# Performance work log

Measured on AMD Instinct MI355X. Metric: run time of the kernel, lower is better.

The kernel has to match this reference:

```python
import jax, jax.numpy as jnp
import numpy as np

NW, OBS, HS, HS2, HM, CTX, ACT = 2048, 512, 512, 512, 256, 128, 18


def setup_inputs() -> dict:
    key = jax.random.key(0)
    ks = jax.random.split(key, 20)
    s = 0.02  # small init so tanh/softmax/sigmoid stay in sane range
    f32 = jnp.float32
    return {
        "obs": jax.random.normal(ks[0], (NW, 1, OBS), f32),
        "hidden_memory": jax.random.normal(ks[1], (1, NW, HM), f32),
        # fnn: Linear(obs_size, hidden_size)
        "W1": (jax.random.normal(ks[2], (HS, OBS), f32) * s),
        "b1": jnp.zeros((HS,), f32),
        # context: Linear(hidden_memory_size + 1, context_size)
        "Wc": (jax.random.normal(ks[3], (CTX, HM + 1), f32) * s),
        "bc": jnp.zeros((CTX,), f32),
        # attention: Linear(context_size, 1)
        "Wa": (jax.random.normal(ks[4], (1, CTX), f32) * s),
        "ba": jnp.zeros((1,), f32),
        # GRU(input=1, hidden=HM)
        "W_ih": (jax.random.normal(ks[5], (3 * HM, 1), f32) * s),
        "b_ih": jnp.zeros((3 * HM,), f32),
        "W_hh": (jax.random.normal(ks[6], (3 * HM, HM), f32) * s),
        "b_hh": jnp.zeros((3 * HM,), f32),
        # fnn2: Linear(hidden_size + hidden_memory_size, hidden_size_2)
        "W2": (jax.random.normal(ks[7], (HS2, HS + HM), f32) * s),
        "b2": jnp.zeros((HS2,), f32),
        # actor / critic heads
        "Wact": (jax.random.normal(ks[8], (ACT, HS2), f32) * s),
        "bact": jnp.zeros((ACT,), f32),
        "Wcrit": (jax.random.normal(ks[9], (1, HS2), f32) * s),
        "bcrit": jnp.zeros((1,), f32),
    }


def reference(obs, hidden_memory, W1, b1, Wc, bc, Wa, ba,
              W_ih, b_ih, W_hh, b_hh, W2, b2, Wact, bact, Wcrit, bcrit):
    # obs: [NW, 1, OBS], hidden_memory: [1, NW, HM]
    feat = jax.nn.relu(jnp.einsum('bto,ho->bth', obs, W1) + b1)  # [NW,1,HS]

    # context: Linear([obs_scalar, hidden_memory]) + tanh.
    # Split the (HM+1)-dim contraction: col 0 multiplies the obs scalar,
    # cols 1: contract with the broadcast hidden memory (same math as the
    # torch cat + Linear, without materializing the [NW,1,OBS,HM+1] tensor).
    h = jnp.swapaxes(hidden_memory, 0, 1)                        # [NW,1,HM]
    h_term = jnp.einsum('btm,cm->btc', h, Wc[:, 1:]) + bc        # [NW,1,CTX]
    ctx = jnp.tanh(obs[..., None] * Wc[:, 0] + h_term[:, :, None, :])  # [NW,1,OBS,CTX]

    # attention: Linear(CTX -> 1) then softmax over the obs dimension (dim=-2
    # of [...,OBS,1] == OBS after squeeze)
    alog = jnp.einsum('btoc,c->bto', ctx, Wa[0]) + ba[0]         # [NW,1,OBS]
    attn = jax.nn.softmax(alog, axis=-1)
    dset = jnp.sum(attn * obs, axis=-1, keepdims=True)           # [NW,1,1]

    # single-step GRU (torch gate ordering: r, z, n)
    x = dset[:, 0, :]                                            # [NW,1]
    hp = hidden_memory[0]                                        # [NW,HM]
    gi = x @ W_ih.T + b_ih                                       # [NW,3HM]
    gh = hp @ W_hh.T + b_hh
    ir, iz, inn = jnp.split(gi, 3, axis=-1)
    hr, hz, hn = jnp.split(gh, 3, axis=-1)
    r = jax.nn.sigmoid(ir + hr)
    z = jax.nn.sigmoid(iz + hz)
    n = jnp.tanh(inn + r * hn)
    hnew = (1.0 - z) * n + z * hp                                # [NW,HM]

    out = jnp.concatenate([feat[:, 0, :], hnew], axis=-1)        # [NW,HS+HM]
    out = jax.nn.relu(out @ W2.T + b2)                           # [NW,HS2]
    logits = out @ Wact.T + bact                                 # [NW,ACT]
    action = jax.random.categorical(jax.random.key(42), logits)  # [NW]
    log_prob = jax.nn.log_softmax(logits)[jnp.arange(logits.shape[0]), action]
    value = out @ Wcrit.T + bcrit                                # [NW,1]
    return (action, value, log_prob)
```

## Files before the change

kernel.cpp:

```cpp
#include <hip/hip_runtime.h>
#include <stdint.h>

#define NW   2048
#define OBS  512
#define HS   512
#define HS2  512
#define HM   256
#define CTX  128
#define ACT  18

#define K2LE 2.8853900817779268f

#define W1T_OFF   0
#define WCT_OFF   262144
#define WHHT_OFF  294912
#define W2T_OFF   491520
#define FEAT_OFF  884736
#define HTERM_OFF 1933312
#define GATES_OFF 2195456
#define OUT2_OFF  2195456
#define HNEW_OFF  3768320

#if __has_builtin(__builtin_amdgcn_exp2f)
#define EXP2F(x) __builtin_amdgcn_exp2f(x)
#else
#define EXP2F(x) exp2f(x)
#endif
#if __has_builtin(__builtin_amdgcn_rcpf)
#define RCPF(x) __builtin_amdgcn_rcpf(x)
#else
#define RCPF(x) (1.0f/(x))
#endif

#define TFR(x0, x1, R) { x0 += x1; x1 = (x1 << R) | (x1 >> (32 - R)); x1 ^= x0; }

__device__ __forceinline__ void threefry_0_42(uint32_t x0, uint32_t x1,
                                              uint32_t& o0, uint32_t& o1) {
    const uint32_t ks0 = 0u;
    const uint32_t ks1 = 42u;
    const uint32_t ks2 = 0x1BD11BDAu ^ ks0 ^ ks1;
    x0 += ks0; x1 += ks1;
    TFR(x0, x1, 13) TFR(x0, x1, 15) TFR(x0, x1, 26) TFR(x0, x1, 6)
    x0 += ks1; x1 += ks2 + 1u;
    TFR(x0, x1, 17) TFR(x0, x1, 29) TFR(x0, x1, 16) TFR(x0, x1, 24)
    x0 += ks2; x1 += ks0 + 2u;
    TFR(x0, x1, 13) TFR(x0, x1, 15) TFR(x0, x1, 26) TFR(x0, x1, 6)
    x0 += ks0; x1 += ks1 + 3u;
    TFR(x0, x1, 17) TFR(x0, x1, 29) TFR(x0, x1, 16) TFR(x0, x1, 24)
    x0 += ks1; x1 += ks2 + 4u;
    TFR(x0, x1, 13) TFR(x0, x1, 15) TFR(x0, x1, 26) TFR(x0, x1, 6)
    x0 += ks2; x1 += ks0 + 5u;
    o0 = x0; o1 = x1;
}

__device__ __forceinline__ float gumbel_ra(int row, int a) {
    uint32_t n = (uint32_t)(row * ACT + a);
    uint32_t o0, o1;
    threefry_0_42(0u, n, o0, o1);
    uint32_t bits = o0 ^ o1;
    uint32_t fb = (bits >> 9) | 0x3F800000u;
    float f = __uint_as_float(fb) - 1.0f;
    const float tiny = 1.17549435e-38f;
    float u = (f < tiny) ? tiny : f;
    return -logf(-logf(u));
}

__device__ __forceinline__ float fast_tanh(float x) {
    float e = __expf(2.0f * x);
    return 1.0f - 2.0f / (e + 1.0f);
}
__device__ __forceinline__ float fast_sig(float x) {
    return 1.0f / (1.0f + __expf(-x));
}
__device__ __forceinline__ void fma4(float4& a, float s, const float4 w) {
    a.x = fmaf(s, w.x, a.x); a.y = fmaf(s, w.y, a.y);
    a.z = fmaf(s, w.z, a.z); a.w = fmaf(s, w.w, a.w);
}

__global__ __launch_bounds__(256) void transpose_weights(
    const float* __restrict__ W1, const float* __restrict__ Wc,
    const float* __restrict__ Whh, const float* __restrict__ W2,
    float* __restrict__ ws)
{
    int b = blockIdx.x;
    const float* src; float* dst; int ld, off, R, it, jt;
    if (b < 256)      { src = W1;  dst = ws + W1T_OFF;  ld = 512; off = 0; it = b >> 4; jt = b & 15; R = 512; }
    else if (b < 288) { b -= 256; src = Wc;  dst = ws + WCT_OFF;  ld = 257; off = 1; it = b >> 3; jt = b & 7;  R = 128; }
    else if (b < 480) { b -= 288; src = Whh; dst = ws + WHHT_OFF; ld = 256; off = 0; it = b / 8;  jt = b % 8;  R = 768; }
    else              { b -= 480; src = W2;  dst = ws + W2T_OFF;  ld = 768; off = 0; it = b / 24; jt = b % 24; R = 512; }
    __shared__ float t[32][33];
    const int tx = threadIdx.x & 31, ty = threadIdx.x >> 5;
    const int i0 = it * 32, j0 = jt * 32;
    #pragma unroll
    for (int q = 0; q < 4; ++q)
        t[ty + 8 * q][tx] = src[(i0 + ty + 8 * q) * ld + off + j0 + tx];
    __syncthreads();
    #pragma unroll
    for (int q = 0; q < 4; ++q)
        dst[(j0 + ty + 8 * q) * R + i0 + tx] = t[tx][ty + 8 * q];
}

__global__ __launch_bounds__(256) void gemm_bcast(
    const float* __restrict__ obs, const float* __restrict__ hmem,
    const float* __restrict__ b1,  const float* __restrict__ bc,
    const float* __restrict__ bhh, float* __restrict__ ws)
{
    __shared__ float s_act[16 * 768];
    float4* P = (float4*)s_act;

    int bid = blockIdx.x;
    const float* A; int lda; const float4* Bt4; int NQ, K, kshift;
    const float* bias; float* C; int ldc; float scale; int act; int rowb, colb;
    if (bid < 512) {
        rowb = bid >> 2; colb = bid & 3;
        A = obs; lda = 512; Bt4 = (const float4*)(ws + W1T_OFF); NQ = 128; K = 512; kshift = 7;
        bias = b1; C = ws + FEAT_OFF; ldc = 512; scale = 1.0f; act = 1;
    } else if (bid < 640) {
        rowb = bid - 512; colb = 0;
        A = hmem; lda = 256; Bt4 = (const float4*)(ws + WCT_OFF); NQ = 32; K = 256; kshift = 6;
        bias = bc; C = ws + HTERM_OFF; ldc = 128; scale = K2LE; act = 0;
    } else {
        int i = bid - 640; rowb = i / 6; colb = i - rowb * 6;
        A = hmem; lda = 256; Bt4 = (const float4*)(ws + WHHT_OFF); NQ = 192; K = 256; kshift = 6;
        bias = bhh; C = ws + GATES_OFF; ldc = 768; scale = 1.0f; act = 0;
    }
    const int m0 = rowb * 16;
    const int kq4 = K >> 2;

    for (int i = threadIdx.x; i < 16 * kq4; i += 256) {
        int r = i >> kshift, kq = i & (kq4 - 1);
        *(float4*)&s_act[r * K + kq * 4] =
            *(const float4*)&A[(size_t)(m0 + r) * lda + kq * 4];
    }
    __syncthreads();

    const int lane = threadIdx.x & 63, wv = threadIdx.x >> 6;
    const int kq2 = lane & 1, c4l = lane >> 1;
    const int kslice = K >> 3;
    const int k0 = (wv * 2 + kq2) * kslice;
    const int cq = colb * 32 + c4l;

    float4 acc[16];
    #pragma unroll
    for (int r = 0; r < 16; ++r) acc[r] = make_float4(0.f, 0.f, 0.f, 0.f);

    #pragma unroll 2
    for (int kk = k0; kk < k0 + kslice; kk += 4) {
        float4 w0 = Bt4[(kk + 0) * NQ + cq];
        float4 w1 = Bt4[(kk + 1) * NQ + cq];
        float4 w2 = Bt4[(kk + 2) * NQ + cq];
        float4 w3 = Bt4[(kk + 3) * NQ + cq];
        #pragma unroll
        for (int r = 0; r < 16; ++r) {
            float4 o = *(const float4*)&s_act[r * K + kk];
            fma4(acc[r], o.x, w0); fma4(acc[r], o.y, w1);
            fma4(acc[r], o.z, w2); fma4(acc[r], o.w, w3);
        }
    }
    #pragma unroll
    for (int r = 0; r < 16; ++r) {
        acc[r].x += __shfl_xor(acc[r].x, 1);
        acc[r].y += __shfl_xor(acc[r].y, 1);
        acc[r].z += __shfl_xor(acc[r].z, 1);
        acc[r].w += __shfl_xor(acc[r].w, 1);
    }
    __syncthreads();
    if (kq2 == 0) {
        #pragma unroll
        for (int r = 0; r < 16; ++r) P[(r * 4 + wv) * 32 + c4l] = acc[r];
    }
    __syncthreads();
    const float4* bias4 = (const float4*)bias;
    for (int s = threadIdx.x; s < 512; s += 256) {
        int r = s >> 5, c = s & 31;
        float4 p0 = P[(r * 4 + 0) * 32 + c];
        float4 p1 = P[(r * 4 + 1) * 32 + c];
        float4 p2 = P[(r * 4 + 2) * 32 + c];
        float4 p3 = P[(r * 4 + 3) * 32 + c];
        float4 bb = bias4[colb * 32 + c];
        float4 v;
        v.x = (p0.x + p1.x + p2.x + p3.x + bb.x) * scale;
        v.y = (p0.y + p1.y + p2.y + p3.y + bb.y) * scale;
        v.z = (p0.z + p1.z + p2.z + p3.z + bb.z) * scale;
        v.w = (p0.w + p1.w + p2.w + p3.w + bb.w) * scale;
        if (act) {
            v.x = fmaxf(v.x, 0.f); v.y = fmaxf(v.y, 0.f);
            v.z = fmaxf(v.z, 0.f); v.w = fmaxf(v.w, 0.f);
        }
        *(float4*)&C[(size_t)(m0 + r) * ldc + (colb * 32 + c) * 4] = v;
    }
}

__global__ __launch_bounds__(512) void attn_gru_kernel(
    const float* __restrict__ obs,  const float* __restrict__ hmem,
    const float* __restrict__ Wc,   const float* __restrict__ Wa,
    const float* __restrict__ ba,   const float* __restrict__ W_ih,
    const float* __restrict__ b_ih, float* __restrict__ ws)
{
    __shared__ float s_obs[8][512];
    __shared__ float s_ht[8][128];
    __shared__ float s_alog[8][512];
    __shared__ float s_wc0[128], s_wa2[128];
    __shared__ float s_x[8];

    const int tid = threadIdx.x;
    const int row0 = blockIdx.x * 8;
    const float* hterm = ws + HTERM_OFF;
    const float* gates = ws + GATES_OFF;
    float* hnew = ws + HNEW_OFF;

    for (int i = tid; i < 1024; i += 512) {
        int r = i >> 7, kq = i & 127;
        *(float4*)&s_obs[r][kq * 4] =
            *(const float4*)&obs[(size_t)(row0 + r) * 512 + kq * 4];
    }
    if (tid < 256) {
        int r = tid >> 5, kq = tid & 31;
        *(float4*)&s_ht[r][kq * 4] =
            *(const float4*)&hterm[(size_t)(row0 + r) * 128 + kq * 4];
    }
    if (tid < 128) {
        s_wc0[tid] = K2LE * Wc[tid * (HM + 1)];
        s_wa2[tid] = 2.0f * Wa[tid];
    }
    __syncthreads();

    {
        const float ba0 = ba[0];
        const int o = tid;
        float ob[8], acA[8];
        #pragma unroll
        for (int r = 0; r < 8; ++r) { ob[r] = s_obs[r][o]; acA[r] = 0.f; }
        float swa = 0.f;
        for (int c = 0; c < 128; c += 4) {
            float4 v = *(const float4*)&s_wa2[c];
            swa += v.x + v.y + v.z + v.w;
        }
        swa *= 0.5f;
        for (int c4 = 0; c4 < 32; ++c4) {
            float4 wc = *(const float4*)&s_wc0[c4 * 4];
            float4 wa = *(const float4*)&s_wa2[c4 * 4];
            #pragma unroll
            for (int r = 0; r < 8; ++r) {
                float4 ht = *(const float4*)&s_ht[r][c4 * 4];
                float t0 = fmaf(ob[r], wc.x, ht.x);
                acA[r] = fmaf(wa.x, RCPF(EXP2F(t0) + 1.f), acA[r]);
                float t1 = fmaf(ob[r], wc.y, ht.y);
                acA[r] = fmaf(wa.y, RCPF(EXP2F(t1) + 1.f), acA[r]);
                float t2 = fmaf(ob[r], wc.z, ht.z);
                acA[r] = fmaf(wa.z, RCPF(EXP2F(t2) + 1.f), acA[r]);
                float t3 = fmaf(ob[r], wc.w, ht.w);
                acA[r] = fmaf(wa.w, RCPF(EXP2F(t3) + 1.f), acA[r]);
            }
        }
        #pragma unroll
        for (int r = 0; r < 8; ++r) s_alog[r][o] = ba0 + swa - acA[r];
    }
    __syncthreads();

    {
        const int wv = tid >> 6, lane = tid & 63;
        const int r = wv;
        float m = -1e30f;
        for (int o = lane; o < 512; o += 64) m = fmaxf(m, s_alog[r][o]);
        #pragma unroll
        for (int d = 32; d >= 1; d >>= 1) m = fmaxf(m, __shfl_xor(m, d));
        float se = 0.f, sw = 0.f;
        for (int o = lane; o < 512; o += 64) {
            float e = __expf(s_alog[r][o] - m);
            se += e; sw += e * s_obs[r][o];
        }
        #pragma unroll
        for (int d = 32; d >= 1; d >>= 1) { se += __shfl_xor(se, d); sw += __shfl_xor(sw, d); }
        if (lane == 0) s_x[r] = sw / se;
    }
    __syncthreads();

    #pragma unroll
    for (int q = 0; q < 4; ++q) {
        int e = tid + q * 512;
        int r = e >> 8, j = e & 255;
        int grow = row0 + r;
        float g0 = gates[(size_t)grow * 768 + j];
        float g1 = gates[(size_t)grow * 768 + 256 + j];
        float g2 = gates[(size_t)grow * 768 + 512 + j];
        float hp = hmem[(size_t)grow * 256 + j];
        float x  = s_x[r];
        float rg = fast_sig(fmaf(x, W_ih[j], b_ih[j]) + g0);
        float zg = fast_sig(fmaf(x, W_ih[256 + j], b_ih[256 + j]) + g1);
        float ng = fast_tanh(fmaf(x, W_ih[512 + j], b_ih[512 + j]) + rg * g2);
        hnew[(size_t)grow * 256 + j] = (1.0f - zg) * ng + zg * hp;
    }
}

__global__ __launch_bounds__(256) void gemm_out2(
    const float* __restrict__ b2, float* __restrict__ ws)
{
    __shared__ float s_act[16 * 768];
    float4* P = (float4*)s_act;

    const int bid = blockIdx.x;
    const int rowb = bid >> 2, colb = bid & 3;
    const int m0 = rowb * 16;
    const float* feat = ws + FEAT_OFF;
    const float* hnew = ws + HNEW_OFF;
    const float4* Bt4 = (const float4*)(ws + W2T_OFF);
    float* C = ws + OUT2_OFF;

    for (int i = threadIdx.x; i < 16 * 192; i += 256) {
        int r = i / 192, kq = i - r * 192;
        float4 v = (kq < 128)
            ? *(const float4*)&feat[(size_t)(m0 + r) * 512 + kq * 4]
            : *(const float4*)&hnew[(size_t)(m0 + r) * 256 + (kq - 128) * 4];
        *(float4*)&s_act[r * 768 + kq * 4] = v;
    }
    __syncthreads();

    const int lane = threadIdx.x & 63, wv = threadIdx.x >> 6;
    const int kq2 = lane & 1, c4l = lane >> 1;
    const int kslice = 96;
    const int k0 = (wv * 2 + kq2) * kslice;
    const int cq = colb * 32 + c4l;

    float4 acc[16];
    #pragma unroll
    for (int r = 0; r < 16; ++r) acc[r] = make_float4(0.f, 0.f, 0.f, 0.f);

    #pragma unroll 2
    for (int kk = k0; kk < k0 + kslice; kk += 4) {
        float4 w0 = Bt4[(kk + 0) * 128 + cq];
        float4 w1 = Bt4[(kk + 1) * 128 + cq];
        float4 w2 = Bt4[(kk + 2) * 128 + cq];
        float4 w3 = Bt4[(kk + 3) * 128 + cq];
        #pragma unroll
        for (int r = 0; r < 16; ++r) {
            float4 o = *(const float4*)&s_act[r * 768 + kk];
            fma4(acc[r], o.x, w0); fma4(acc[r], o.y, w1);
            fma4(acc[r], o.z, w2); fma4(acc[r], o.w, w3);
        }
    }
    #pragma unroll
    for (int r = 0; r < 16; ++r) {
        acc[r].x += __shfl_xor(acc[r].x, 1);
        acc[r].y += __shfl_xor(acc[r].y, 1);
        acc[r].z += __shfl_xor(acc[r].z, 1);
        acc[r].w += __shfl_xor(acc[r].w, 1);
    }
    __syncthreads();
    if (kq2 == 0) {
        #pragma unroll
        for (int r = 0; r < 16; ++r) P[(r * 4 + wv) * 32 + c4l] = acc[r];
    }
    __syncthreads();
    const float4* bias4 = (const float4*)b2;
    for (int s = threadIdx.x; s < 512; s += 256) {
        int r = s >> 5, c = s & 31;
        float4 p0 = P[(r * 4 + 0) * 32 + c];
        float4 p1 = P[(r * 4 + 1) * 32 + c];
        float4 p2 = P[(r * 4 + 2) * 32 + c];
        float4 p3 = P[(r * 4 + 3) * 32 + c];
        float4 bb = bias4[colb * 32 + c];
        float4 v;
        v.x = fmaxf(p0.x + p1.x + p2.x + p3.x + bb.x, 0.f);
        v.y = fmaxf(p0.y + p1.y + p2.y + p3.y + bb.y, 0.f);
        v.z = fmaxf(p0.z + p1.z + p2.z + p3.z + bb.z, 0.f);
        v.w = fmaxf(p0.w + p1.w + p2.w + p3.w + bb.w, 0.f);
        *(float4*)&C[(size_t)(m0 + r) * 512 + (colb * 32 + c) * 4] = v;
    }
}

__global__ __launch_bounds__(512) void heads_kernel(
    const float* __restrict__ Wact,  const float* __restrict__ bact,
    const float* __restrict__ Wcrit, const float* __restrict__ bcrit,
    const float* __restrict__ ws,    float* __restrict__ out)
{
    const int wv = threadIdx.x >> 6, lane = threadIdx.x & 63;
    const int grow = blockIdx.x * 8 + wv;
    const float* o2 = ws + OUT2_OFF;

    float4 x0 = *(const float4*)&o2[(size_t)grow * 512 + lane * 8];
    float4 x1 = *(const float4*)&o2[(size_t)grow * 512 + lane * 8 + 4];

    float la[ACT];
    #pragma unroll
    for (int a = 0; a < ACT; ++a) {
        const float4* wa4 = (const float4*)&Wact[a * HS2 + lane * 8];
        float4 w0 = wa4[0], w1 = wa4[1];
        float p = x0.x * w0.x + x0.y * w0.y + x0.z * w0.z + x0.w * w0.w
                + x1.x * w1.x + x1.y * w1.y + x1.z * w1.z + x1.w * w1.w;
        #pragma unroll
        for (int d = 32; d >= 1; d >>= 1) p += __shfl_xor(p, d);
        la[a] = p + bact[a];
    }
    const float4* wc4 = (const float4*)&Wcrit[lane * 8];
    float4 w0 = wc4[0], w1 = wc4[1];
    float pv = x0.x * w0.x + x0.y * w0.y + x0.z * w0.z + x0.w * w0.w
             + x1.x * w1.x + x1.y * w1.y + x1.z * w1.z + x1.w * w1.w;
    #pragma unroll
    for (int d = 32; d >= 1; d >>= 1) pv += __shfl_xor(pv, d);

    float g = (lane < ACT) ? gumbel_ra(grow, lane) : 0.0f;
    float best = -1e30f; int amax = 0;
    float mx = -1e30f;
    #pragma unroll
    for (int a = 0; a < ACT; ++a) {
        float g_ = __shfl(g, a);
        float y = la[a] + g_;
        if (y > best) { best = y; amax = a; }
        mx = fmaxf(mx, la[a]);
    }
    float se = 0.f;
    #pragma unroll
    for (int a = 0; a < ACT; ++a) se += __expf(la[a] - mx);
    float lse = mx + logf(se);
    float lp = la[amax] - lse;
    if (lane == 0) {
        out[grow]          = (float)amax;
        out[NW + grow]     = pv + bcrit[0];
        out[2 * NW + grow] = lp;
    }
}

extern "C" void kernel_launch(void* const* d_in, const int* in_sizes, int n_in,
                              void* d_out, int out_size, void* d_ws, size_t ws_size,
                              hipStream_t stream) {
    const float* obs   = (const float*)d_in[0];
    const float* hmem  = (const float*)d_in[1];
    const float* W1    = (const float*)d_in[2];
    const float* b1    = (const float*)d_in[3];
    const float* Wc    = (const float*)d_in[4];
    const float* bc    = (const float*)d_in[5];
    const float* Wa    = (const float*)d_in[6];
    const float* ba    = (const float*)d_in[7];
    const float* W_ih  = (const float*)d_in[8];
    const float* b_ih  = (const float*)d_in[9];
    const float* W_hh  = (const float*)d_in[10];
    const float* b_hh  = (const float*)d_in[11];
    const float* W2    = (const float*)d_in[12];
    const float* b2    = (const float*)d_in[13];
    const float* Wact  = (const float*)d_in[14];
    const float* bact  = (const float*)d_in[15];
    const float* Wcrit = (const float*)d_in[16];
    const float* bcrit = (const float*)d_in[17];
    float* ws = (float*)d_ws;

    transpose_weights<<<864, 256, 0, stream>>>(W1, Wc, W_hh, W2, ws);
    gemm_bcast<<<1408, 256, 0, stream>>>(obs, hmem, b1, bc, b_hh, ws);
    attn_gru_kernel<<<256, 512, 0, stream>>>(obs, hmem, Wc, Wa, ba, W_ih, b_ih, ws);
    gemm_out2<<<512, 256, 0, stream>>>(b2, ws);
    heads_kernel<<<256, 512, 0, stream>>>(Wact, bact, Wcrit, bcrit, ws, (float*)d_out);
}
```

Measured before the change: 128.7 us.

## Fuse GRU update, out2 GEMM and heads; retile GEMMs to 8-row blocks

The GRU gate update moves out of the attention kernel and into a new fused kernel that also computes the out2 GEMM and the actor/critic heads. This removes the hnew and out2 round trips through global memory and cuts one launch. The GEMMs are retiled to 8 rows per block, with each thread owning whole output columns over the full K range, so the cross-wave split-K reduction through shared memory goes away. W_hh is repacked into an interleaved r/z/n float4 layout so one load feeds all three gates. The cost is more per-thread K iterations, less parallelism per block, and fewer blocks in the fused final kernel.

Result: slower. 137.5 us (+6.9%).

```diff
diff --git a/kernel.cpp b/kernel.cpp
--- a/kernel.cpp
+++ b/kernel.cpp
@@ -13,13 +13,12 @@
 
 #define W1T_OFF   0
 #define WCT_OFF   262144
-#define WHHT_OFF  294912
-#define W2T_OFF   491520
-#define FEAT_OFF  884736
-#define HTERM_OFF 1933312
-#define GATES_OFF 2195456
-#define OUT2_OFF  2195456
-#define HNEW_OFF  3768320
+#define W2T_OFF   294912
+#define WHHQ_OFF  688128
+#define FEAT_OFF  950272
+#define GATES_OFF 1998848
+#define HTERM_OFF 3571712
+#define X_OFF     3833856
 
 #if __has_builtin(__builtin_amdgcn_exp2f)
 #define EXP2F(x) __builtin_amdgcn_exp2f(x)
@@ -72,142 +71,182 @@
 __device__ __forceinline__ float fast_sig(float x) {
     return 1.0f / (1.0f + __expf(-x));
 }
-__device__ __forceinline__ void fma4(float4& a, float s, const float4 w) {
-    a.x = fmaf(s, w.x, a.x); a.y = fmaf(s, w.y, a.y);
-    a.z = fmaf(s, w.z, a.z); a.w = fmaf(s, w.w, a.w);
-}
 
 __global__ __launch_bounds__(256) void transpose_weights(
     const float* __restrict__ W1, const float* __restrict__ Wc,
     const float* __restrict__ Whh, const float* __restrict__ W2,
     float* __restrict__ ws)
 {
+    __shared__ float t[3][32][33];
+    const int tx = threadIdx.x & 31, ty = threadIdx.x >> 5;
     int b = blockIdx.x;
-    const float* src; float* dst; int ld, off, R, it, jt;
-    if (b < 256)      { src = W1;  dst = ws + W1T_OFF;  ld = 512; off = 0; it = b >> 4; jt = b & 15; R = 512; }
-    else if (b < 288) { b -= 256; src = Wc;  dst = ws + WCT_OFF;  ld = 257; off = 1; it = b >> 3; jt = b & 7;  R = 128; }
-    else if (b < 480) { b -= 288; src = Whh; dst = ws + WHHT_OFF; ld = 256; off = 0; it = b / 8;  jt = b % 8;  R = 768; }
-    else              { b -= 480; src = W2;  dst = ws + W2T_OFF;  ld = 768; off = 0; it = b / 24; jt = b % 24; R = 512; }
-    __shared__ float t[32][33];
-    const int tx = threadIdx.x & 31, ty = threadIdx.x >> 5;
-    const int i0 = it * 32, j0 = jt * 32;
-    #pragma unroll
-    for (int q = 0; q < 4; ++q)
-        t[ty + 8 * q][tx] = src[(i0 + ty + 8 * q) * ld + off + j0 + tx];
-    __syncthreads();
-    #pragma unroll
-    for (int q = 0; q < 4; ++q)
-        dst[(j0 + ty + 8 * q) * R + i0 + tx] = t[tx][ty + 8 * q];
-}
-
-__global__ __launch_bounds__(256) void gemm_bcast(
+    if (b < 672) {
+        const float* src; float* dst; int ld, off, R, it, jt;
+        if (b < 256)      { src = W1;  dst = ws + W1T_OFF;  ld = 512; off = 0; it = b >> 4; jt = b & 15; R = 512; }
+        else if (b < 288) { int bb = b - 256; src = Wc;  dst = ws + WCT_OFF;  ld = 257; off = 1; it = bb >> 3; jt = bb & 7;  R = 128; }
+        else              { int bb = b - 288; src = W2;  dst = ws + W2T_OFF;  ld = 768; off = 0; it = bb / 24; jt = bb % 24; R = 512; }
+        const int i0 = it * 32, j0 = jt * 32;
+        #pragma unroll
+        for (int q = 0; q < 4; ++q)
+            t[0][ty + 8 * q][tx] = src[(i0 + ty + 8 * q) * ld + off + j0 + tx];
+        __syncthreads();
+        #pragma unroll
+        for (int q = 0; q < 4; ++q)
+            dst[(j0 + ty + 8 * q) * R + i0 + tx] = t[0][tx][ty + 8 * q];
+    } else {
+        int bb = b - 672;
+        const int mt = bb >> 3, jt = bb & 7;
+        const int m0 = mt * 32, j0 = jt * 32;
+        #pragma unroll
+        for (int g = 0; g < 3; ++g)
+            #pragma unroll
+            for (int q = 0; q < 4; ++q)
+                t[g][ty + 8 * q][tx] = Whh[(g * HM + j0 + ty + 8 * q) * HM + m0 + tx];
+        __syncthreads();
+        float4* dst = (float4*)(ws + WHHQ_OFF);
+        #pragma unroll
+        for (int q = 0; q < 4; ++q) {
+            int ml = ty + 8 * q, jl = tx;
+            dst[(size_t)(m0 + ml) * HM + j0 + jl] =
+                make_float4(t[0][jl][ml], t[1][jl][ml], t[2][jl][ml], 0.0f);
+        }
+    }
+}
+
+__global__ __launch_bounds__(256) void gemm8(
     const float* __restrict__ obs, const float* __restrict__ hmem,
     const float* __restrict__ b1,  const float* __restrict__ bc,
     const float* __restrict__ bhh, float* __restrict__ ws)
 {
-    __shared__ float s_act[16 * 768];
-    float4* P = (float4*)s_act;
-
-    int bid = blockIdx.x;
-    const float* A; int lda; const float4* Bt4; int NQ, K, kshift;
-    const float* bias; float* C; int ldc; float scale; int act; int rowb, colb;
-    if (bid < 512) {
-        rowb = bid >> 2; colb = bid & 3;
-        A = obs; lda = 512; Bt4 = (const float4*)(ws + W1T_OFF); NQ = 128; K = 512; kshift = 7;
-        bias = b1; C = ws + FEAT_OFF; ldc = 512; scale = 1.0f; act = 1;
-    } else if (bid < 640) {
-        rowb = bid - 512; colb = 0;
-        A = hmem; lda = 256; Bt4 = (const float4*)(ws + WCT_OFF); NQ = 32; K = 256; kshift = 6;
-        bias = bc; C = ws + HTERM_OFF; ldc = 128; scale = K2LE; act = 0;
+    __shared__ float s_act[8 * 512];
+    const int tid = threadIdx.x;
+    const int wv = tid >> 6, lane = tid & 63;
+    const int bid = blockIdx.x;
+
+    if (bid < 256) {
+        const int m0 = bid * 8;
+        for (int i = tid; i < 1024; i += 256) {
+            int r = i >> 7, kq = i & 127;
+            *(float4*)&s_act[r * 512 + kq * 4] =
+                *(const float4*)&obs[(size_t)(m0 + r) * 512 + kq * 4];
+        }
+        __syncthreads();
+        const float2* __restrict__ Wt = (const float2*)(ws + W1T_OFF);
+        const int c2 = wv * 64 + lane;
+        float2 acc[8];
+        #pragma unroll
+        for (int r = 0; r < 8; ++r) acc[r] = make_float2(0.f, 0.f);
+        #pragma unroll 2
+        for (int k = 0; k < 512; k += 4) {
+            float2 w0 = Wt[(k + 0) * 256 + c2];
+            float2 w1 = Wt[(k + 1) * 256 + c2];
+            float2 w2 = Wt[(k + 2) * 256 + c2];
+            float2 w3 = Wt[(k + 3) * 256 + c2];
+            #pragma unroll
+            for (int r = 0; r < 8; ++r) {
+                float4 o = *(const float4*)&s_act[r * 512 + k];
+                acc[r].x = fmaf(o.x, w0.x, acc[r].x); acc[r].y = fmaf(o.x, w0.y, acc[r].y);
+                acc[r].x = fmaf(o.y, w1.x, acc[r].x); acc[r].y = fmaf(o.y, w1.y, acc[r].y);
+                acc[r].x = fmaf(o.z, w2.x, acc[r].x); acc[r].y = fmaf(o.z, w2.y, acc[r].y);
+                acc[r].x = fmaf(o.w, w3.x, acc[r].x); acc[r].y = fmaf(o.w, w3.y, acc[r].y);
+            }
+        }
+        float2 bb = ((const float2*)b1)[c2];
+        float* F = ws + FEAT_OFF;
+        #pragma unroll
+        for (int r = 0; r < 8; ++r) {
+            float2 v;
+            v.x = fmaxf(acc[r].x + bb.x, 0.f);
+            v.y = fmaxf(acc[r].y + bb.y, 0.f);
+            *(float2*)&F[(size_t)(m0 + r) * 512 + c2 * 2] = v;
+        }
+    } else if (bid < 512) {
+        const int m0 = (bid - 256) * 8;
+        for (int i = tid; i < 512; i += 256) {
+            int r = i >> 6, kq = i & 63;
+            *(float4*)&s_act[r * 256 + kq * 4] =
+                *(const float4*)&hmem[(size_t)(m0 + r) * 256 + kq * 4];
+        }
+        __syncthreads();
+        const float4* __restrict__ Q = (const float4*)(ws + WHHQ_OFF);
+        const int j = wv * 64 + lane;
+        float ar[8] = {0,0,0,0,0,0,0,0}, az[8] = {0,0,0,0,0,0,0,0}, an[8] = {0,0,0,0,0,0,0,0};
+        #pragma unroll 2
+        for (int k = 0; k < 256; k += 4) {
+            float4 q0 = Q[(k + 0) * 256 + j];
+            float4 q1 = Q[(k + 1) * 256 + j];
+            float4 q2 = Q[(k + 2) * 256 + j];
+            float4 q3 = Q[(k + 3) * 256 + j];
+            #pragma unroll
+            for (int r = 0; r < 8; ++r) {
+                float4 h = *(const float4*)&s_act[r * 256 + k];
+                ar[r] = fmaf(h.x, q0.x, ar[r]); az[r] = fmaf(h.x, q0.y, az[r]); an[r] = fmaf(h.x, q0.z, an[r]);
+                ar[r] = fmaf(h.y, q1.x, ar[r]); az[r] = fmaf(h.y, q1.y, az[r]); an[r] = fmaf(h.y, q1.z, an[r]);
+                ar[r] = fmaf(h.z, q2.x, ar[r]); az[r] = fmaf(h.z, q2.y, az[r]); an[r] = fmaf(h.z, q2.z, an[r]);
+                ar[r] = fmaf(h.w, q3.x, ar[r]); az[r] = fmaf(h.w, q3.y, az[r]); an[r] = fmaf(h.w, q3.z, an[r]);
+            }
+        }
+        float br = bhh[j], bz = bhh[HM + j], bn = bhh[2 * HM + j];
+        float* G = ws + GATES_OFF;
+        #pragma unroll
+        for (int r = 0; r < 8; ++r) {
+            size_t base = (size_t)(m0 + r) * 768 + j;
+            G[base]       = ar[r] + br;
+            G[base + 256] = az[r] + bz;
+            G[base + 512] = an[r] + bn;
+        }
     } else {
-        int i = bid - 640; rowb = i / 6; colb = i - rowb * 6;
-        A = hmem; lda = 256; Bt4 = (const float4*)(ws + WHHT_OFF); NQ = 192; K = 256; kshift = 6;
-        bias = bhh; C = ws + GATES_OFF; ldc = 768; scale = 1.0f; act = 0;
-    }
-    const int m0 = rowb * 16;
-    const int kq4 = K >> 2;
-
-    for (int i = threadIdx.x; i < 16 * kq4; i += 256) {
-        int r = i >> kshift, kq = i & (kq4 - 1);
-        *(float4*)&s_act[r * K + kq * 4] =
-            *(const float4*)&A[(size_t)(m0 + r) * lda + kq * 4];
-    }
-    __syncthreads();
-
-    const int lane = threadIdx.x & 63, wv = threadIdx.x >> 6;
-    const int kq2 = lane & 1, c4l = lane >> 1;
-    const int kslice = K >> 3;
-    const int k0 = (wv * 2 + kq2) * kslice;
-    const int cq = colb * 32 + c4l;
-
-    float4 acc[16];
-    #pragma unroll
-    for (int r = 0; r < 16; ++r) acc[r] = make_float4(0.f, 0.f, 0.f, 0.f);
-
-    #pragma unroll 2
-    for (int kk = k0; kk < k0 + kslice; kk += 4) {
-        float4 w0 = Bt4[(kk + 0) * NQ + cq];
-        float4 w1 = Bt4[(kk + 1) * NQ + cq];
-        float4 w2 = Bt4[(kk + 2) * NQ + cq];
-        float4 w3 = Bt4[(kk + 3) * NQ + cq];
-        #pragma unroll
-        for (int r = 0; r < 16; ++r) {
-            float4 o = *(const float4*)&s_act[r * K + kk];
-            fma4(acc[r], o.x, w0); fma4(acc[r], o.y, w1);
-            fma4(acc[r], o.z, w2); fma4(acc[r], o.w, w3);
-        }
-    }
-    #pragma unroll
-    for (int r = 0; r < 16; ++r) {
-        acc[r].x += __shfl_xor(acc[r].x, 1);
-        acc[r].y += __shfl_xor(acc[r].y, 1);
-        acc[r].z += __shfl_xor(acc[r].z, 1);
-        acc[r].w += __shfl_xor(acc[r].w, 1);
-    }
-    __syncthreads();
-    if (kq2 == 0) {
-        #pragma unroll
-        for (int r = 0; r < 16; ++r) P[(r * 4 + wv) * 32 + c4l] = acc[r];
-    }
-    __syncthreads();
-    const float4* bias4 = (const float4*)bias;
-    for (int s = threadIdx.x; s < 512; s += 256) {
-        int r = s >> 5, c = s & 31;
-        float4 p0 = P[(r * 4 + 0) * 32 + c];
-        float4 p1 = P[(r * 4 + 1) * 32 + c];
-        float4 p2 = P[(r * 4 + 2) * 32 + c];
-        float4 p3 = P[(r * 4 + 3) * 32 + c];
-        float4 bb = bias4[colb * 32 + c];
-        float4 v;
-        v.x = (p0.x + p1.x + p2.x + p3.x + bb.x) * scale;
-        v.y = (p0.y + p1.y + p2.y + p3.y + bb.y) * scale;
-        v.z = (p0.z + p1.z + p2.z + p3.z + bb.z) * scale;
-        v.w = (p0.w + p1.w + p2.w + p3.w + bb.w) * scale;
-        if (act) {
-            v.x = fmaxf(v.x, 0.f); v.y = fmaxf(v.y, 0.f);
-            v.z = fmaxf(v.z, 0.f); v.w = fmaxf(v.w, 0.f);
-        }
-        *(float4*)&C[(size_t)(m0 + r) * ldc + (colb * 32 + c) * 4] = v;
-    }
-}
-
-__global__ __launch_bounds__(512) void attn_gru_kernel(
-    const float* __restrict__ obs,  const float* __restrict__ hmem,
-    const float* __restrict__ Wc,   const float* __restrict__ Wa,
-    const float* __restrict__ ba,   const float* __restrict__ W_ih,
-    const float* __restrict__ b_ih, float* __restrict__ ws)
+        const int m0 = (bid - 512) * 8;
+        for (int i = tid; i < 512; i += 256) {
+            int r = i >> 6, kq = i & 63;
+            *(float4*)&s_act[r * 256 + kq * 4] =
+                *(const float4*)&hmem[(size_t)(m0 + r) * 256 + kq * 4];
+        }
+        __syncthreads();
+        const float2* __restrict__ Wt = (const float2*)(ws + WCT_OFF);
+        const int r0 = wv * 2;
+        float2 a0 = make_float2(0.f, 0.f), a1 = make_float2(0.f, 0.f);
+        #pragma unroll 2
+        for (int k = 0; k < 256; k += 4) {
+            float2 w0 = Wt[(k + 0) * 64 + lane];
+            float2 w1 = Wt[(k + 1) * 64 + lane];
+            float2 w2 = Wt[(k + 2) * 64 + lane];
+            float2 w3 = Wt[(k + 3) * 64 + lane];
+            float4 o0 = *(const float4*)&s_act[r0 * 256 + k];
+            float4 o1 = *(const float4*)&s_act[(r0 + 1) * 256 + k];
+            a0.x = fmaf(o0.x, w0.x, a0.x); a0.y = fmaf(o0.x, w0.y, a0.y);
+            a0.x = fmaf(o0.y, w1.x, a0.x); a0.y = fmaf(o0.y, w1.y, a0.y);
+            a0.x = fmaf(o0.z, w2.x, a0.x); a0.y = fmaf(o0.z, w2.y, a0.y);
+            a0.x = fmaf(o0.w, w3.x, a0.x); a0.y = fmaf(o0.w, w3.y, a0.y);
+            a1.x = fmaf(o1.x, w0.x, a1.x); a1.y = fmaf(o1.x, w0.y, a1.y);
+            a1.x = fmaf(o1.y, w1.x, a1.x); a1.y = fmaf(o1.y, w1.y, a1.y);
+            a1.x = fmaf(o1.z, w2.x, a1.x); a1.y = fmaf(o1.z, w2.y, a1.y);
+            a1.x = fmaf(o1.w, w3.x, a1.x); a1.y = fmaf(o1.w, w3.y, a1.y);
+        }
+        float2 bb = ((const float2*)bc)[lane];
+        float* H = ws + HTERM_OFF;
+        float2 v0, v1;
+        v0.x = K2LE * (a0.x + bb.x); v0.y = K2LE * (a0.y + bb.y);
+        v1.x = K2LE * (a1.x + bb.x); v1.y = K2LE * (a1.y + bb.y);
+        *(float2*)&H[(size_t)(m0 + r0) * 128 + lane * 2]     = v0;
+        *(float2*)&H[(size_t)(m0 + r0 + 1) * 128 + lane * 2] = v1;
+    }
+}
+
+__global__ __launch_bounds__(512) void attn_kernel(
+    const float* __restrict__ obs, const float* __restrict__ Wc,
+    const float* __restrict__ Wa,  const float* __restrict__ ba,
+    float* __restrict__ ws)
 {
     __shared__ float s_obs[8][512];
     __shared__ float s_ht[8][128];
     __shared__ float s_alog[8][512];
     __shared__ float s_wc0[128], s_wa2[128];
-    __shared__ float s_x[8];
 
     const int tid = threadIdx.x;
     const int row0 = blockIdx.x * 8;
     const float* hterm = ws + HTERM_OFF;
-    const float* gates = ws + GATES_OFF;
-    float* hnew = ws + HNEW_OFF;
+    float* X = ws + X_OFF;
 
     for (int i = tid; i < 1024; i += 512) {
         int r = i >> 7, kq = i & 127;
@@ -272,152 +311,119 @@
         }
         #pragma unroll
         for (int d = 32; d >= 1; d >>= 1) { se += __shfl_xor(se, d); sw += __shfl_xor(sw, d); }
-        if (lane == 0) s_x[r] = sw / se;
-    }
-    __syncthreads();
-
-    #pragma unroll
-    for (int q = 0; q < 4; ++q) {
-        int e = tid + q * 512;
-        int r = e >> 8, j = e & 255;
-        int grow = row0 + r;
-        float g0 = gates[(size_t)grow * 768 + j];
-        float g1 = gates[(size_t)grow * 768 + 256 + j];
-        float g2 = gates[(size_t)grow * 768 + 512 + j];
-        float hp = hmem[(size_t)grow * 256 + j];
-        float x  = s_x[r];
-        float rg = fast_sig(fmaf(x, W_ih[j], b_ih[j]) + g0);
-        float zg = fast_sig(fmaf(x, W_ih[256 + j], b_ih[256 + j]) + g1);
-        float ng = fast_tanh(fmaf(x, W_ih[512 + j], b_ih[512 + j]) + rg * g2);
-        hnew[(size_t)grow * 256 + j] = (1.0f - zg) * ng + zg * hp;
-    }
-}
-
-__global__ __launch_bounds__(256) void gemm_out2(
-    const float* __restrict__ b2, float* __restrict__ ws)
-{
-    __shared__ float s_act[16 * 768];
-    float4* P = (float4*)s_act;
-
-    const int bid = blockIdx.x;
-    const int rowb = bid >> 2, colb = bid & 3;
-    const int m0 = rowb * 16;
-    const float* feat = ws + FEAT_OFF;
-    const float* hnew = ws + HNEW_OFF;
-    const float4* Bt4 = (const float4*)(ws + W2T_OFF);
-    float* C = ws + OUT2_OFF;
-
-    for (int i = threadIdx.x; i < 16 * 192; i += 256) {
-        int r = i / 192, kq = i - r * 192;
-        float4 v = (kq < 128)
-            ? *(const float4*)&feat[(size_t)(m0 + r) * 512 + kq * 4]
-            : *(const float4*)&hnew[(size_t)(m0 + r) * 256 + (kq - 128) * 4];
-        *(float4*)&s_act[r * 768 + kq * 4] = v;
-    }
-    __syncthreads();
-
-    const int lane = threadIdx.x & 63, wv = threadIdx.x >> 6;
-    const int kq2 = lane & 1, c4l = lane >> 1;
-    const int kslice = 96;
-    const int k0 = (wv * 2 + kq2) * kslice;
-    const int cq = colb * 32 + c4l;
-
-    float4 acc[16];
-    #pragma unroll
-    for (int r = 0; r < 16; ++r) acc[r] = make_float4(0.f, 0.f, 0.f, 0.f);
-
-    #pragma unroll 2
-    for (int kk = k0; kk < k0 + kslice; kk += 4) {
-        float4 w0 = Bt4[(kk + 0) * 128 + cq];
-        float4 w1 = Bt4[(kk + 1) * 128 + cq];
-        float4 w2 = Bt4[(kk + 2) * 128 + cq];
-        float4 w3 = Bt4[(kk + 3) * 128 + cq];
-        #pragma unroll
-        for (int r = 0; r < 16; ++r) {
-            float4 o = *(const float4*)&s_act[r * 768 + kk];
-            fma4(acc[r], o.x, w0); fma4(acc[r], o.y, w1);
-            fma4(acc[r], o.z, w2); fma4(acc[r], o.w, w3);
-        }
-    }
-    #pragma unroll
-    for (int r = 0; r < 16; ++r) {
-        acc[r].x += __shfl_xor(acc[r].x, 1);
-        acc[r].y += __shfl_xor(acc[r].y, 1);
-        acc[r].z += __shfl_xor(acc[r].z, 1);
-        acc[r].w += __shfl_xor(acc[r].w, 1);
-    }
-    __syncthreads();
-    if (kq2 == 0) {
-        #pragma unroll
-        for (int r = 0; r < 16; ++r) P[(r * 4 + wv) * 32 + c4l] = acc[r];
-    }
-    __syncthreads();
-    const float4* bias4 = (const float4*)b2;
-    for (int s = threadIdx.x; s < 512; s += 256) {
-        int r = s >> 5, c = s & 31;
-        float4 p0 = P[(r * 4 + 0) * 32 + c];
-        float4 p1 = P[(r * 4 + 1) * 32 + c];
-        float4 p2 = P[(r * 4 + 2) * 32 + c];
-        float4 p3 = P[(r * 4 + 3) * 32 + c];
-        float4 bb = bias4[colb * 32 + c];
-        float4 v;
-        v.x = fmaxf(p0.x + p1.x + p2.x + p3.x + bb.x, 0.f);
-        v.y = fmaxf(p0.y + p1.y + p2.y + p3.y + bb.y, 0.f);
-        v.z = fmaxf(p0.z + p1.z + p2.z + p3.z + bb.z, 0.f);
-        v.w = fmaxf(p0.w + p1.w + p2.w + p3.w + bb.w, 0.f);
-        *(float4*)&C[(size_t)(m0 + r) * 512 + (colb * 32 + c) * 4] = v;
-    }
-}
-
-__global__ __launch_bounds__(512) void heads_kernel(
+        if (lane == 0) X[row0 + r] = sw / se;
+    }
+}
+
+__global__ __launch_bounds__(256) void out2_heads(
+    const float* __restrict__ hmem,  const float* __restrict__ W_ih,
+    const float* __restrict__ b_ih,  const float* __restrict__ b2,
     const float* __restrict__ Wact,  const float* __restrict__ bact,
     const float* __restrict__ Wcrit, const float* __restrict__ bcrit,
     const float* __restrict__ ws,    float* __restrict__ out)
 {
-    const int wv = threadIdx.x >> 6, lane = threadIdx.x & 63;
-    const int grow = blockIdx.x * 8 + wv;
-    const float* o2 = ws + OUT2_OFF;
-
-    float4 x0 = *(const float4*)&o2[(size_t)grow * 512 + lane * 8];
-    float4 x1 = *(const float4*)&o2[(size_t)grow * 512 + lane * 8 + 4];
-
-    float la[ACT];
+    __shared__ float s_act[8 * 768];
+    const int tid = threadIdx.x;
+    const int wv = tid >> 6, lane = tid & 63;
+    const int m0 = blockIdx.x * 8;
+    const float* F = ws + FEAT_OFF;
+    const float* G = ws + GATES_OFF;
+    const float* X = ws + X_OFF;
+
+    for (int i = tid; i < 1024; i += 256) {
+        int r = i >> 7, kq = i & 127;
+        *(float4*)&s_act[r * 768 + kq * 4] =
+            *(const float4*)&F[(size_t)(m0 + r) * 512 + kq * 4];
+    }
+    for (int i = tid; i < 2048; i += 256) {
+        int r = i >> 8, j = i & 255;
+        int grow = m0 + r;
+        float g0 = G[(size_t)grow * 768 + j];
+        float g1 = G[(size_t)grow * 768 + 256 + j];
+        float g2 = G[(size_t)grow * 768 + 512 + j];
+        float hp = hmem[(size_t)grow * 256 + j];
+        float x  = X[grow];
+        float rg = fast_sig(fmaf(x, W_ih[j], b_ih[j]) + g0);
+        float zg = fast_sig(fmaf(x, W_ih[256 + j], b_ih[256 + j]) + g1);
+        float ng = fast_tanh(fmaf(x, W_ih[512 + j], b_ih[512 + j]) + rg * g2);
+        s_act[r * 768 + 512 + j] = (1.0f - zg) * ng + zg * hp;
+    }
+    __syncthreads();
+
+    const float2* __restrict__ Wt = (const float2*)(ws + W2T_OFF);
+    const int c2 = wv * 64 + lane;
+    float2 acc[8];
     #pragma unroll
-    for (int a = 0; a < ACT; ++a) {
-        const float4* wa4 = (const float4*)&Wact[a * HS2 + lane * 8];
-        float4 w0 = wa4[0], w1 = wa4[1];
-        float p = x0.x * w0.x + x0.y * w0.y + x0.z * w0.z + x0.w * w0.w
-                + x1.x * w1.x + x1.y * w1.y + x1.z * w1.z + x1.w * w1.w;
-        #pragma unroll
-        for (int d = 32; d >= 1; d >>= 1) p += __shfl_xor(p, d);
-        la[a] = p + bact[a];
-    }
-    const float4* wc4 = (const float4*)&Wcrit[lane * 8];
-    float4 w0 = wc4[0], w1 = wc4[1];
-    float pv = x0.x * w0.x + x0.y * w0.y + x0.z * w0.z + x0.w * w0.w
-             + x1.x * w1.x + x1.y * w1.y + x1.z * w1.z + x1.w * w1.w;
+    for (int r = 0; r < 8; ++r) acc[r] = make_float2(0.f, 0.f);
+    #pragma unroll 2
+    for (int k = 0; k < 768; k += 4) {
+        float2 w0 = Wt[(k + 0) * 256 + c2];
+        float2 w1 = Wt[(k + 1) * 256 + c2];
+        float2 w2 = Wt[(k + 2) * 256 + c2];
+        float2 w3 = Wt[(k + 3) * 256 + c2];
+        #pragma unroll
+        for (int r = 0; r < 8; ++r) {
+            float4 o = *(const float4*)&s_act[r * 768 + k];
+            acc[r].x = fmaf(o.x, w0.x, acc[r].x); acc[r].y = fmaf(o.x, w0.y, acc[r].y);
+            acc[r].x = fmaf(o.y, w1.x, acc[r].x); acc[r].y = fmaf(o.y, w1.y, acc[r].y);
+            acc[r].x = fmaf(o.z, w2.x, acc[r].x); acc[r].y = fmaf(o.z, w2.y, acc[r].y);
+            acc[r].x = fmaf(o.w, w3.x, acc[r].x); acc[r].y = fmaf(o.w, w3.y, acc[r].y);
+        }
+    }
+    float2 bb = ((const float2*)b2)[c2];
+    __syncthreads();
+    float (*s_out)[512] = (float (*)[512])s_act;
     #pragma unroll
-    for (int d = 32; d >= 1; d >>= 1) pv += __shfl_xor(pv, d);
-
-    float g = (lane < ACT) ? gumbel_ra(grow, lane) : 0.0f;
-    float best = -1e30f; int amax = 0;
-    float mx = -1e30f;
-    #pragma unroll
-    for (int a = 0; a < ACT; ++a) {
-        float g_ = __shfl(g, a);
-        float y = la[a] + g_;
-        if (y > best) { best = y; amax = a; }
-        mx = fmaxf(mx, la[a]);
-    }
-    float se = 0.f;
-    #pragma unroll
-    for (int a = 0; a < ACT; ++a) se += __expf(la[a] - mx);
-    float lse = mx + logf(se);
-    float lp = la[amax] - lse;
-    if (lane == 0) {
-        out[grow]          = (float)amax;
-        out[NW + grow]     = pv + bcrit[0];
-        out[2 * NW + grow] = lp;
+    for (int r = 0; r < 8; ++r) {
+        float2 v;
+        v.x = fmaxf(acc[r].x + bb.x, 0.f);
+        v.y = fmaxf(acc[r].y + bb.y, 0.f);
+        *(float2*)&s_out[r][c2 * 2] = v;
+    }
+    __syncthreads();
+
+    for (int rr = wv; rr < 8; rr += 4) {
+        const int grow = m0 + rr;
+        float4 x0 = *(const float4*)&s_out[rr][lane * 8];
+        float4 x1 = *(const float4*)&s_out[rr][lane * 8 + 4];
+        float la[ACT];
+        #pragma unroll
+        for (int a = 0; a < ACT; ++a) {
+            const float4* wa4 = (const float4*)&Wact[a * HS2 + lane * 8];
+            float4 w0 = wa4[0], w1 = wa4[1];
+            float p = x0.x * w0.x + x0.y * w0.y + x0.z * w0.z + x0.w * w0.w
+                    + x1.x * w1.x + x1.y * w1.y + x1.z * w1.z + x1.w * w1.w;
+            #pragma unroll
+            for (int d = 32; d >= 1; d >>= 1) p += __shfl_xor(p, d);
+            la[a] = p + bact[a];
+        }
+        const float4* wc4 = (const float4*)&Wcrit[lane * 8];
+        float4 w0 = wc4[0], w1 = wc4[1];
+        float pv = x0.x * w0.x + x0.y * w0.y + x0.z * w0.z + x0.w * w0.w
+                 + x1.x * w1.x + x1.y * w1.y + x1.z * w1.z + x1.w * w1.w;
+        #pragma unroll
+        for (int d = 32; d >= 1; d >>= 1) pv += __shfl_xor(pv, d);
+
+        float g = (lane < ACT) ? gumbel_ra(grow, lane) : 0.0f;
+        float best = -1e30f; int amax = 0;
+        float mx = -1e30f;
+        #pragma unroll
+        for (int a = 0; a < ACT; ++a) {
+            float g_ = __shfl(g, a);
+            float y = la[a] + g_;
+            if (y > best) { best = y; amax = a; }
+            mx = fmaxf(mx, la[a]);
+        }
+        float se = 0.f;
+        #pragma unroll
+        for (int a = 0; a < ACT; ++a) se += __expf(la[a] - mx);
+        float lse = mx + logf(se);
+        float lp = la[amax] - lse;
+        if (lane == 0) {
+            out[grow]          = (float)amax;
+            out[NW + grow]     = pv + bcrit[0];
+            out[2 * NW + grow] = lp;
+        }
     }
 }
 
@@ -444,9 +450,9 @@
     const float* bcrit = (const float*)d_in[17];
     float* ws = (float*)d_ws;
 
-    transpose_weights<<<864, 256, 0, stream>>>(W1, Wc, W_hh, W2, ws);
-    gemm_bcast<<<1408, 256, 0, stream>>>(obs, hmem, b1, bc, b_hh, ws);
-    attn_gru_kernel<<<256, 512, 0, stream>>>(obs, hmem, Wc, Wa, ba, W_ih, b_ih, ws);
-    gemm_out2<<<512, 256, 0, stream>>>(b2, ws);
-    heads_kernel<<<256, 512, 0, stream>>>(Wact, bact, Wcrit, bcrit, ws, (float*)d_out);
-}
+    transpose_weights<<<736, 256, 0, stream>>>(W1, Wc, W_hh, W2, ws);
+    gemm8<<<768, 256, 0, stream>>>(obs, hmem, b1, bc, b_hh, ws);
+    attn_kernel<<<256, 512, 0, stream>>>(obs, Wc, Wa, ba, ws);
+    out2_heads<<<256, 256, 0, stream>>>(hmem, W_ih, b_ih, b2,
+                                        Wact, bact, Wcrit, bcrit, ws, (float*)d_out);
+}
```
